# Kernel tuning notes

Measured on AMD Instinct MI355X. Metric: run time of the kernel, lower is better.

The kernel has to match this reference:

```python
import jax, jax.numpy as jnp
import numpy as np

B, T, C = 4, 2048, 1024
E, K, HID = 8, 2, 4096  # n_expert, top-k, mult*dim


def setup_inputs() -> dict:
    key = jax.random.key(0)
    ks = jax.random.split(key, 9)
    s = 1.0 / np.sqrt(C)
    sh = 1.0 / np.sqrt(HID)
    return {
        "x": jax.random.normal(ks[0], (B, T, C), jnp.float32),
        "wg_w": jax.random.normal(ks[1], (C, E), jnp.float32) * s,
        "wg_b": jnp.zeros((E,), jnp.float32),
        "w1": jax.random.normal(ks[2], (E, C, HID), jnp.float32) * s,
        "b1": jnp.zeros((E, HID), jnp.float32),
        "w3": jax.random.normal(ks[3], (E, C, HID), jnp.float32) * s,
        "b3": jnp.zeros((E, HID), jnp.float32),
        "w2": jax.random.normal(ks[4], (E, HID, C), jnp.float32) * sh,
        "b2": jnp.zeros((E, C), jnp.float32),
    }


def reference(x, wg_w, wg_b, w1, b1, w3, b3, w2, b2):
    Bx, Tx, Cx = x.shape
    xf = x.reshape(-1, Cx)                       # (S, C)
    S = xf.shape[0]
    # --- TopKGate ---
    logits = xf @ wg_w + wg_b                    # (S, E)
    probs = jax.nn.softmax(logits, axis=-1)
    vals, idx = jax.lax.top_k(probs, K)          # (S, K)
    importance = probs.mean(axis=0)              # (E,)
    load = jnp.zeros((E,), probs.dtype).at[idx[:, 0]].add(1.0) / S
    aux = E * (importance * load).sum()
    # per-token per-expert combine weight (top-k ids are unique per row)
    w_full = jnp.zeros((S, E), probs.dtype).at[jnp.arange(S)[:, None], idx].add(vals)
    # --- experts: SwiGLU FFN, loop over small fixed E ---
    y = jnp.zeros_like(xf)
    for e in range(E):
        h = jax.nn.silu(xf @ w1[e] + b1[e]) * (xf @ w3[e] + b3[e])  # (S, HID)
        y = y + w_full[:, e:e + 1] * (h @ w2[e] + b2[e])
    return y.reshape(Bx, Tx, Cx), aux
```

## Files before the change

### kernel.cpp

```cpp
#include <hip/hip_runtime.h>

#define S_TOK 8192
#define C_DIM 1024
#define E_NUM 8
#define HID_DIM 4096

typedef unsigned short u16;
typedef __bf16 bf16x8 __attribute__((ext_vector_type(8)));
typedef float f32x4 __attribute__((ext_vector_type(4)));

__device__ __forceinline__ u16 f2bf(float f){
  union { float f; unsigned u; } v; v.f = f;
  unsigned r = v.u + 0x7fffu + ((v.u >> 16) & 1u);
  return (u16)(r >> 16);
}
__device__ __forceinline__ float bf2f(u16 b){
  union { unsigned u; float f; } v; v.u = ((unsigned)b) << 16; return v.f;
}

__device__ __forceinline__ void async_copy16(const void* g, void* l){
  __builtin_amdgcn_global_load_lds((const __attribute__((address_space(1))) void*)g,
                                   (__attribute__((address_space(3))) void*)l, 16, 0, 0);
}

__global__ __launch_bounds__(256) void gate_kernel(
    const float* __restrict__ x, const float* __restrict__ wg_w, const float* __restrict__ wg_b,
    int* __restrict__ top_idx, float* __restrict__ top_val,
    float* __restrict__ imp_sum, int* __restrict__ cnt_top1, int* __restrict__ counts)
{
  __shared__ float s_imp[E_NUM];
  __shared__ int   s_c1[E_NUM], s_cnt[E_NUM];
  if (threadIdx.x < E_NUM){ s_imp[threadIdx.x]=0.f; s_c1[threadIdx.x]=0; s_cnt[threadIdx.x]=0; }
  __syncthreads();

  int wid = threadIdx.x >> 6, lane = threadIdx.x & 63;
  int t = blockIdx.x * 4 + wid;
  const float4* xr4 = (const float4*)(x + (size_t)t * C_DIM);
  float acc[E_NUM];
  #pragma unroll
  for (int e=0;e<E_NUM;e++) acc[e]=0.f;
  #pragma unroll
  for (int c4 = 0; c4 < C_DIM/4/64; c4++){
    int c = (c4*64 + lane);
    float4 xv = xr4[c];
    const float* wr = wg_w + (size_t)c * 4 * E_NUM;
    #pragma unroll
    for (int e=0;e<E_NUM;e++)
      acc[e] += xv.x*wr[e] + xv.y*wr[E_NUM+e] + xv.z*wr[2*E_NUM+e] + xv.w*wr[3*E_NUM+e];
  }
  #pragma unroll
  for (int e=0;e<E_NUM;e++){
    float v = acc[e];
    #pragma unroll
    for (int off=32; off>0; off>>=1) v += __shfl_xor(v, off, 64);
    acc[e] = v + wg_b[e];
  }
  float mx = acc[0];
  #pragma unroll
  for (int e=1;e<E_NUM;e++) mx = fmaxf(mx, acc[e]);
  float sum = 0.f;
  #pragma unroll
  for (int e=0;e<E_NUM;e++){ acc[e] = __expf(acc[e]-mx); sum += acc[e]; }
  float inv = 1.f/sum;
  #pragma unroll
  for (int e=0;e<E_NUM;e++) acc[e] *= inv;
  int i1=0; float v1=acc[0];
  #pragma unroll
  for (int e=1;e<E_NUM;e++) if (acc[e] > v1){ v1=acc[e]; i1=e; }
  int i2=-1; float v2=-1.f;
  #pragma unroll
  for (int e=0;e<E_NUM;e++) if (e!=i1 && acc[e] > v2){ v2=acc[e]; i2=e; }

  if (lane==0){
    top_idx[t*2+0]=i1; top_idx[t*2+1]=i2;
    top_val[t*2+0]=v1; top_val[t*2+1]=v2;
    #pragma unroll
    for (int e=0;e<E_NUM;e++) atomicAdd(&s_imp[e], acc[e]);
    atomicAdd(&s_c1[i1],1);
    atomicAdd(&s_cnt[i1],1); atomicAdd(&s_cnt[i2],1);
  }
  __syncthreads();
  if (threadIdx.x < E_NUM){
    atomicAdd(&imp_sum[threadIdx.x], s_imp[threadIdx.x]);
    atomicAdd(&cnt_top1[threadIdx.x], s_c1[threadIdx.x]);
    atomicAdd(&counts[threadIdx.x], s_cnt[threadIdx.x]);
  }
}

__global__ void scan_kernel(const int* __restrict__ counts, int* __restrict__ offsets,
                            int* __restrict__ cursor, const float* __restrict__ imp_sum,
                            const int* __restrict__ cnt_top1, float* __restrict__ aux_out)
{
  if (threadIdx.x==0 && blockIdx.x==0){
    int off=0;
    #pragma unroll
    for (int e=0;e<E_NUM;e++){ offsets[e]=off; cursor[e]=off; off+=counts[e]; }
    float aux=0.f;
    #pragma unroll
    for (int e=0;e<E_NUM;e++)
      aux += (imp_sum[e]/(float)S_TOK) * ((float)cnt_top1[e]/(float)S_TOK);
    aux_out[0] = aux * (float)E_NUM;
  }
}

__global__ __launch_bounds__(256) void scatter_kernel(
    const int* __restrict__ top_idx, const float* __restrict__ top_val,
    int* __restrict__ cursor, int* __restrict__ token_list, float* __restrict__ token_w,
    int* __restrict__ pos_of_slot)
{
  int t = blockIdx.x*256 + threadIdx.x;
  #pragma unroll
  for (int k=0;k<2;k++){
    int e = top_idx[t*2+k];
    int pos = atomicAdd(&cursor[e], 1);
    token_list[pos] = t;
    token_w[pos]    = top_val[t*2+k];
    pos_of_slot[t*2+k] = pos;
  }
}

__global__ __launch_bounds__(256) void convx_kernel(const float* __restrict__ x, u16* __restrict__ xb){
  const int n4 = S_TOK*C_DIM/4;
  for (int i = blockIdx.x*blockDim.x + threadIdx.x; i < n4; i += gridDim.x*blockDim.x){
    float4 v = ((const float4*)x)[i];
    ushort4 o = make_ushort4(f2bf(v.x), f2bf(v.y), f2bf(v.z), f2bf(v.w));
    ((ushort4*)xb)[i] = o;
  }
}

__global__ __launch_bounds__(256) void transpose_kernel(const float* __restrict__ in, u16* __restrict__ out,
                                                        int R, int Cc)
{
  __shared__ float tile[64][65];
  int e = blockIdx.z;
  const float* src = in  + (size_t)e*R*Cc;
  u16*         dst = out + (size_t)e*R*Cc;
  int c0 = blockIdx.x*64, r0 = blockIdx.y*64;
  int tx = threadIdx.x, ty = threadIdx.y;
  #pragma unroll
  for (int i = ty; i < 64; i += 4)
    tile[i][tx] = src[(size_t)(r0+i)*Cc + c0 + tx];
  __syncthreads();
  #pragma unroll
  for (int i = ty; i < 64; i += 4)
    dst[(size_t)(c0+i)*R + r0 + tx] = f2bf(tile[tx][i]);
}

__global__ __launch_bounds__(512,1) void gemm1_kernel(
    const u16* __restrict__ xb, const u16* __restrict__ w1t, const u16* __restrict__ w3t,
    const float* __restrict__ b1, const float* __restrict__ b3,
    const int* __restrict__ token_list, const int* __restrict__ offsets, const int* __restrict__ counts,
    u16* __restrict__ h)
{
  int e  = blockIdx.z;
  int Ne = counts[e];
  int m0 = blockIdx.y * 128;
  if (m0 >= Ne) return;
  int seg = offsets[e];
  int n0  = blockIdx.x * 128;

  __shared__ u16 lA [128*64];
  __shared__ u16 lB1[128*64];
  __shared__ u16 lB3[128*64];

  int tid = threadIdx.x;
  int wid = tid >> 6, lane = tid & 63;
  int wr = wid >> 2, wc = wid & 3;

  size_t gA[2], gB[2];
  #pragma unroll
  for (int i=0;i<2;i++){
    int r  = wid*16 + i*8 + (lane>>3);
    int rr = m0 + r; if (rr > Ne-1) rr = Ne-1;
    int tok = token_list[seg + rr];
    gA[i] = (size_t)tok * C_DIM + (lane&7)*8;
    int n  = n0 + wid*16 + i*8 + (lane>>3);
    gB[i] = ((size_t)e*HID_DIM + n) * C_DIM + (lane&7)*8;
  }

  f32x4 acc1[4][2], acc3[4][2];
  #pragma unroll
  for (int a=0;a<4;a++)
    #pragma unroll
    for (int b=0;b<2;b++){ acc1[a][b] = (f32x4){0.f,0.f,0.f,0.f}; acc3[a][b] = (f32x4){0.f,0.f,0.f,0.f}; }

  for (int k0=0; k0<C_DIM; k0+=64){
    #pragma unroll
    for (int i=0;i<2;i++){
      int lds_off = (wid*16 + i*8) * 64;
      async_copy16(xb  + gA[i] + k0, &lA [lds_off]);
      async_copy16(w1t + gB[i] + k0, &lB1[lds_off]);
      async_copy16(w3t + gB[i] + k0, &lB3[lds_off]);
    }
    __syncthreads();
    #pragma unroll
    for (int ks=0; ks<2; ks++){
      int kk = ks*32 + (lane>>4)*8;
      bf16x8 af[4], b1f[2], b3f[2];
      #pragma unroll
      for (int mi=0;mi<4;mi++) af[mi]  = *(const bf16x8*)&lA [(wr*64+mi*16+(lane&15))*64 + kk];
      #pragma unroll
      for (int nj=0;nj<2;nj++){ b1f[nj] = *(const bf16x8*)&lB1[(wc*32+nj*16+(lane&15))*64 + kk];
                                b3f[nj] = *(const bf16x8*)&lB3[(wc*32+nj*16+(lane&15))*64 + kk]; }
      #pragma unroll
      for (int mi=0;mi<4;mi++)
        #pragma unroll
        for (int nj=0;nj<2;nj++){
          acc1[mi][nj] = __builtin_amdgcn_mfma_f32_16x16x32_bf16(af[mi], b1f[nj], acc1[mi][nj], 0,0,0);
          acc3[mi][nj] = __builtin_amdgcn_mfma_f32_16x16x32_bf16(af[mi], b3f[nj], acc3[mi][nj], 0,0,0);
        }
    }
    __syncthreads();
  }

  const float* b1p = b1 + (size_t)e*HID_DIM + n0;
  const float* b3p = b3 + (size_t)e*HID_DIM + n0;
  #pragma unroll
  for (int nj=0;nj<2;nj++){
    int nl = wc*32 + nj*16 + (lane&15);
    float bb1 = b1p[nl], bb3 = b3p[nl];
    #pragma unroll
    for (int mi=0;mi<4;mi++){
      #pragma unroll
      for (int r=0;r<4;r++){
        int ml = wr*64 + mi*16 + (lane>>4)*4 + r;
        int m  = m0 + ml;
        if (m < Ne){
          float a = acc1[mi][nj][r] + bb1;
          float b = acc3[mi][nj][r] + bb3;
          float hv = (a / (1.f + __expf(-a))) * b;
          h[(size_t)(seg+m)*HID_DIM + n0 + nl] = f2bf(hv);
        }
      }
    }
  }
}

__global__ __launch_bounds__(256,2) void gemm2_kernel(
    const u16* __restrict__ h, const u16* __restrict__ w2t, const float* __restrict__ b2,
    const float* __restrict__ token_w,
    const int* __restrict__ offsets, const int* __restrict__ counts,
    float* __restrict__ ybuf)
{
  int e  = blockIdx.z;
  int Ne = counts[e];
  int m0 = blockIdx.y * 128;
  if (m0 >= Ne) return;
  int seg = offsets[e];
  int n0  = blockIdx.x * 128;

  __shared__ u16 lA[128*64];
  __shared__ u16 lB[128*64];
  int tid=threadIdx.x, wid=tid>>6, lane=tid&63, wr=wid>>1, wc=wid&1;

  size_t gA[4];
  #pragma unroll
  for (int i=0;i<4;i++){
    int r  = wid*32 + i*8 + (lane>>3);
    int rr = m0 + r; if (rr > Ne-1) rr = Ne-1;
    gA[i] = (size_t)(seg + rr)*HID_DIM + (lane&7)*8;
  }
  size_t gB = ((size_t)e*C_DIM + n0 + wid*32 + (lane>>3)) * HID_DIM + (lane&7)*8;

  f32x4 acc[4][4];
  #pragma unroll
  for (int a=0;a<4;a++)
    #pragma unroll
    for (int b=0;b<4;b++) acc[a][b] = (f32x4){0.f,0.f,0.f,0.f};

  for (int k0=0; k0<HID_DIM; k0+=64){
    #pragma unroll
    for (int i=0;i<4;i++){
      async_copy16(h   + gA[i] + k0,                     &lA[(wid*4+i)*512]);
      async_copy16(w2t + gB + (size_t)i*8*HID_DIM + k0,  &lB[(wid*4+i)*512]);
    }
    __syncthreads();
    #pragma unroll
    for (int ks=0; ks<2; ks++){
      int kk = ks*32 + (lane>>4)*8;
      bf16x8 af[4], bf[4];
      #pragma unroll
      for (int mi=0;mi<4;mi++) af[mi] = *(const bf16x8*)&lA[(wr*64+mi*16+(lane&15))*64 + kk];
      #pragma unroll
      for (int nj=0;nj<4;nj++) bf[nj] = *(const bf16x8*)&lB[(wc*64+nj*16+(lane&15))*64 + kk];
      #pragma unroll
      for (int mi=0;mi<4;mi++)
        #pragma unroll
        for (int nj=0;nj<4;nj++)
          acc[mi][nj] = __builtin_amdgcn_mfma_f32_16x16x32_bf16(af[mi], bf[nj], acc[mi][nj], 0,0,0);
    }
    __syncthreads();
  }

  const float* b2p = b2 + (size_t)e*C_DIM + n0;
  #pragma unroll
  for (int mi=0;mi<4;mi++){
    #pragma unroll
    for (int r=0;r<4;r++){
      int ml = wr*64 + mi*16 + (lane>>4)*4 + r;
      int m  = m0 + ml;
      if (m < Ne){
        float w = token_w[seg+m];
        #pragma unroll
        for (int nj=0;nj<4;nj++){
          int nl = wc*64 + nj*16 + (lane&15);
          ybuf[(size_t)(seg+m)*C_DIM + n0 + nl] = (acc[mi][nj][r] + b2p[nl]) * w;
        }
      }
    }
  }
}

__global__ __launch_bounds__(256) void combine_kernel(
    const float* __restrict__ ybuf, const int* __restrict__ pos_of_slot, float* __restrict__ y)
{
  int t = blockIdx.x;
  int p0 = pos_of_slot[t*2+0], p1 = pos_of_slot[t*2+1];
  const float4* a = (const float4*)(ybuf + (size_t)p0*C_DIM);
  const float4* b = (const float4*)(ybuf + (size_t)p1*C_DIM);
  float4* o = (float4*)(y + (size_t)t*C_DIM);
  int c = threadIdx.x;
  float4 va = a[c], vb = b[c];
  o[c] = make_float4(va.x+vb.x, va.y+vb.y, va.z+vb.z, va.w+vb.w);
}

extern "C" void kernel_launch(void* const* d_in, const int* in_sizes, int n_in,
                              void* d_out, int out_size, void* d_ws, size_t ws_size,
                              hipStream_t stream)
{
  const float* x    = (const float*)d_in[0];
  const float* wg_w = (const float*)d_in[1];
  const float* wg_b = (const float*)d_in[2];
  const float* w1   = (const float*)d_in[3];
  const float* b1   = (const float*)d_in[4];
  const float* w3   = (const float*)d_in[5];
  const float* b3   = (const float*)d_in[6];
  const float* w2   = (const float*)d_in[7];
  const float* b2   = (const float*)d_in[8];

  float* y   = (float*)d_out;
  float* aux = y + (size_t)S_TOK*C_DIM;

  char* ws = (char*)d_ws;
  size_t off = 0;
  auto alloc = [&](size_t bytes) -> void* {
    void* p = ws + off;
    off += (bytes + 255) & ~(size_t)255;
    return p;
  };
  u16*  xb        = (u16*)  alloc((size_t)S_TOK*C_DIM*2);
  u16*  w1t       = (u16*)  alloc((size_t)E_NUM*HID_DIM*C_DIM*2);
  u16*  w3t       = (u16*)  alloc((size_t)E_NUM*HID_DIM*C_DIM*2);
  u16*  w2t       = (u16*)  alloc((size_t)E_NUM*C_DIM*HID_DIM*2);
  u16*  h         = (u16*)  alloc((size_t)S_TOK*2*HID_DIM*2);
  int*  token_list= (int*)  alloc((size_t)S_TOK*2*4);
  float* token_w  = (float*)alloc((size_t)S_TOK*2*4);
  int*  top_idx   = (int*)  alloc((size_t)S_TOK*2*4);
  float* top_val  = (float*)alloc((size_t)S_TOK*2*4);
  int*  pos_of_slot=(int*)  alloc((size_t)S_TOK*2*4);
  char* stats     = (char*) alloc(4096);
  float* imp_sum  = (float*)(stats);
  int*   cnt1     = (int*)  (stats + 64);
  int*   counts   = (int*)  (stats + 128);
  int*   offsets  = (int*)  (stats + 192);
  int*   cursor   = (int*)  (stats + 256);
  float* ybuf = (float*)w1t;
  (void)in_sizes; (void)n_in; (void)out_size; (void)ws_size;

  hipMemsetAsync(stats, 0, 512, stream);

  convx_kernel<<<2048, 256, 0, stream>>>(x, xb);
  dim3 tb(64,4);
  transpose_kernel<<<dim3(HID_DIM/64, C_DIM/64, E_NUM), tb, 0, stream>>>(w1, w1t, C_DIM, HID_DIM);
  transpose_kernel<<<dim3(HID_DIM/64, C_DIM/64, E_NUM), tb, 0, stream>>>(w3, w3t, C_DIM, HID_DIM);
  transpose_kernel<<<dim3(C_DIM/64, HID_DIM/64, E_NUM), tb, 0, stream>>>(w2, w2t, HID_DIM, C_DIM);

  gate_kernel<<<S_TOK/4, 256, 0, stream>>>(x, wg_w, wg_b, top_idx, top_val, imp_sum, cnt1, counts);
  scan_kernel<<<1, 64, 0, stream>>>(counts, offsets, cursor, imp_sum, cnt1, aux);
  scatter_kernel<<<S_TOK/256, 256, 0, stream>>>(top_idx, top_val, cursor, token_list, token_w, pos_of_slot);

  gemm1_kernel<<<dim3(HID_DIM/128, S_TOK/128, E_NUM), 512, 0, stream>>>(
      xb, w1t, w3t, b1, b3, token_list, offsets, counts, h);
  gemm2_kernel<<<dim3(C_DIM/128, S_TOK/128, E_NUM), 256, 0, stream>>>(
      h, w2t, b2, token_w, offsets, counts, ybuf);
  combine_kernel<<<S_TOK, 256, 0, stream>>>(ybuf, pos_of_slot, y);
}
```

Measured before the change: 931.8 us.

## Swizzle LDS tiles, widen gemm2 to 8 waves, bf16 ybuf, vectorize transpose

The gemm1 and gemm2 LDS tiles now use an XOR swizzle. It is applied to the global source offset of each async copy and to the k-offset of each fragment read, to cut LDS bank conflicts on the bf16x8 loads. gemm2 moves from 4 waves with 4x4 MFMA tiles to 8 waves with 4x2 tiles, one block per CU. The intermediate expert outputs are stored as bf16 instead of fp32, which halves ybuf traffic in gemm2 and combine at some cost in precision. The weight transpose uses float2 loads and ushort2 stores with a 32x8 thread block.

New measurement: 831.8 us. 10.7% less time.

```diff
diff --git a/kernel.cpp b/kernel.cpp
--- a/kernel.cpp
+++ b/kernel.cpp
@@ -138,13 +138,18 @@
   int c0 = blockIdx.x*64, r0 = blockIdx.y*64;
   int tx = threadIdx.x, ty = threadIdx.y;
   #pragma unroll
-  for (int i = ty; i < 64; i += 4)
-    tile[i][tx] = src[(size_t)(r0+i)*Cc + c0 + tx];
+  for (int i = ty; i < 64; i += 8){
+    float2 v = *(const float2*)&src[(size_t)(r0+i)*Cc + c0 + tx*2];
+    tile[i][tx*2+0] = v.x; tile[i][tx*2+1] = v.y;
+  }
   __syncthreads();
   #pragma unroll
-  for (int i = ty; i < 64; i += 4)
-    dst[(size_t)(c0+i)*R + r0 + tx] = f2bf(tile[tx][i]);
-}
+  for (int i = ty; i < 64; i += 8){
+    ushort2 o = make_ushort2(f2bf(tile[tx*2+0][i]), f2bf(tile[tx*2+1][i]));
+    *(ushort2*)&dst[(size_t)(c0+i)*R + r0 + tx*2] = o;
+  }
+}
+
 
 __global__ __launch_bounds__(512,1) void gemm1_kernel(
     const u16* __restrict__ xb, const u16* __restrict__ w1t, const u16* __restrict__ w3t,
@@ -167,15 +172,17 @@
   int wid = tid >> 6, lane = tid & 63;
   int wr = wid >> 2, wc = wid & 3;
 
+  const int srcsw = (((lane&7) ^ ((lane>>3)&7))) * 8;
+
   size_t gA[2], gB[2];
   #pragma unroll
   for (int i=0;i<2;i++){
     int r  = wid*16 + i*8 + (lane>>3);
     int rr = m0 + r; if (rr > Ne-1) rr = Ne-1;
     int tok = token_list[seg + rr];
-    gA[i] = (size_t)tok * C_DIM + (lane&7)*8;
+    gA[i] = (size_t)tok * C_DIM + srcsw;
     int n  = n0 + wid*16 + i*8 + (lane>>3);
-    gB[i] = ((size_t)e*HID_DIM + n) * C_DIM + (lane&7)*8;
+    gB[i] = ((size_t)e*HID_DIM + n) * C_DIM + srcsw;
   }
 
   f32x4 acc1[4][2], acc3[4][2];
@@ -195,13 +202,13 @@
     __syncthreads();
     #pragma unroll
     for (int ks=0; ks<2; ks++){
-      int kk = ks*32 + (lane>>4)*8;
+      int kkS = ((ks*4 + (lane>>4)) ^ (lane&7)) * 8;
       bf16x8 af[4], b1f[2], b3f[2];
       #pragma unroll
-      for (int mi=0;mi<4;mi++) af[mi]  = *(const bf16x8*)&lA [(wr*64+mi*16+(lane&15))*64 + kk];
-      #pragma unroll
-      for (int nj=0;nj<2;nj++){ b1f[nj] = *(const bf16x8*)&lB1[(wc*32+nj*16+(lane&15))*64 + kk];
-                                b3f[nj] = *(const bf16x8*)&lB3[(wc*32+nj*16+(lane&15))*64 + kk]; }
+      for (int mi=0;mi<4;mi++) af[mi]  = *(const bf16x8*)&lA [(wr*64+mi*16+(lane&15))*64 + kkS];
+      #pragma unroll
+      for (int nj=0;nj<2;nj++){ b1f[nj] = *(const bf16x8*)&lB1[(wc*32+nj*16+(lane&15))*64 + kkS];
+                                b3f[nj] = *(const bf16x8*)&lB3[(wc*32+nj*16+(lane&15))*64 + kkS]; }
       #pragma unroll
       for (int mi=0;mi<4;mi++)
         #pragma unroll
@@ -236,11 +243,11 @@
   }
 }
 
-__global__ __launch_bounds__(256,2) void gemm2_kernel(
+__global__ __launch_bounds__(512,1) void gemm2_kernel(
     const u16* __restrict__ h, const u16* __restrict__ w2t, const float* __restrict__ b2,
     const float* __restrict__ token_w,
     const int* __restrict__ offsets, const int* __restrict__ counts,
-    float* __restrict__ ybuf)
+    u16* __restrict__ ybuf)
 {
   int e  = blockIdx.z;
   int Ne = counts[e];
@@ -251,42 +258,46 @@
 
   __shared__ u16 lA[128*64];
   __shared__ u16 lB[128*64];
-  int tid=threadIdx.x, wid=tid>>6, lane=tid&63, wr=wid>>1, wc=wid&1;
-
-  size_t gA[4];
-  #pragma unroll
-  for (int i=0;i<4;i++){
-    int r  = wid*32 + i*8 + (lane>>3);
+  int tid=threadIdx.x, wid=tid>>6, lane=tid&63, wr=wid>>2, wc=wid&3;
+
+  const int srcsw = (((lane&7) ^ ((lane>>3)&7))) * 8;
+
+  size_t gA[2], gB[2];
+  #pragma unroll
+  for (int i=0;i<2;i++){
+    int r  = wid*16 + i*8 + (lane>>3);
     int rr = m0 + r; if (rr > Ne-1) rr = Ne-1;
-    gA[i] = (size_t)(seg + rr)*HID_DIM + (lane&7)*8;
-  }
-  size_t gB = ((size_t)e*C_DIM + n0 + wid*32 + (lane>>3)) * HID_DIM + (lane&7)*8;
-
-  f32x4 acc[4][4];
+    gA[i] = (size_t)(seg + rr)*HID_DIM + srcsw;
+    int n  = n0 + wid*16 + i*8 + (lane>>3);
+    gB[i] = ((size_t)e*C_DIM + n) * HID_DIM + srcsw;
+  }
+
+  f32x4 acc[4][2];
   #pragma unroll
   for (int a=0;a<4;a++)
     #pragma unroll
-    for (int b=0;b<4;b++) acc[a][b] = (f32x4){0.f,0.f,0.f,0.f};
+    for (int b=0;b<2;b++) acc[a][b] = (f32x4){0.f,0.f,0.f,0.f};
 
   for (int k0=0; k0<HID_DIM; k0+=64){
     #pragma unroll
-    for (int i=0;i<4;i++){
-      async_copy16(h   + gA[i] + k0,                     &lA[(wid*4+i)*512]);
-      async_copy16(w2t + gB + (size_t)i*8*HID_DIM + k0,  &lB[(wid*4+i)*512]);
+    for (int i=0;i<2;i++){
+      int lds_off = (wid*16 + i*8) * 64;
+      async_copy16(h   + gA[i] + k0, &lA[lds_off]);
+      async_copy16(w2t + gB[i] + k0, &lB[lds_off]);
     }
     __syncthreads();
     #pragma unroll
     for (int ks=0; ks<2; ks++){
-      int kk = ks*32 + (lane>>4)*8;
-      bf16x8 af[4], bf[4];
-      #pragma unroll
-      for (int mi=0;mi<4;mi++) af[mi] = *(const bf16x8*)&lA[(wr*64+mi*16+(lane&15))*64 + kk];
-      #pragma unroll
-      for (int nj=0;nj<4;nj++) bf[nj] = *(const bf16x8*)&lB[(wc*64+nj*16+(lane&15))*64 + kk];
+      int kkS = ((ks*4 + (lane>>4)) ^ (lane&7)) * 8;
+      bf16x8 af[4], bf[2];
+      #pragma unroll
+      for (int mi=0;mi<4;mi++) af[mi] = *(const bf16x8*)&lA[(wr*64+mi*16+(lane&15))*64 + kkS];
+      #pragma unroll
+      for (int nj=0;nj<2;nj++) bf[nj] = *(const bf16x8*)&lB[(wc*32+nj*16+(lane&15))*64 + kkS];
       #pragma unroll
       for (int mi=0;mi<4;mi++)
         #pragma unroll
-        for (int nj=0;nj<4;nj++)
+        for (int nj=0;nj<2;nj++)
           acc[mi][nj] = __builtin_amdgcn_mfma_f32_16x16x32_bf16(af[mi], bf[nj], acc[mi][nj], 0,0,0);
     }
     __syncthreads();
@@ -302,9 +313,9 @@
       if (m < Ne){
         float w = token_w[seg+m];
         #pragma unroll
-        for (int nj=0;nj<4;nj++){
-          int nl = wc*64 + nj*16 + (lane&15);
-          ybuf[(size_t)(seg+m)*C_DIM + n0 + nl] = (acc[mi][nj][r] + b2p[nl]) * w;
+        for (int nj=0;nj<2;nj++){
+          int nl = wc*32 + nj*16 + (lane&15);
+          ybuf[(size_t)(seg+m)*C_DIM + n0 + nl] = f2bf((acc[mi][nj][r] + b2p[nl]) * w);
         }
       }
     }
@@ -312,16 +323,16 @@
 }
 
 __global__ __launch_bounds__(256) void combine_kernel(
-    const float* __restrict__ ybuf, const int* __restrict__ pos_of_slot, float* __restrict__ y)
+    const u16* __restrict__ ybuf, const int* __restrict__ pos_of_slot, float* __restrict__ y)
 {
   int t = blockIdx.x;
   int p0 = pos_of_slot[t*2+0], p1 = pos_of_slot[t*2+1];
-  const float4* a = (const float4*)(ybuf + (size_t)p0*C_DIM);
-  const float4* b = (const float4*)(ybuf + (size_t)p1*C_DIM);
-  float4* o = (float4*)(y + (size_t)t*C_DIM);
   int c = threadIdx.x;
-  float4 va = a[c], vb = b[c];
-  o[c] = make_float4(va.x+vb.x, va.y+vb.y, va.z+vb.z, va.w+vb.w);
+  ushort4 a = ((const ushort4*)(ybuf + (size_t)p0*C_DIM))[c];
+  ushort4 b = ((const ushort4*)(ybuf + (size_t)p1*C_DIM))[c];
+  float4 o = make_float4(bf2f(a.x)+bf2f(b.x), bf2f(a.y)+bf2f(b.y),
+                         bf2f(a.z)+bf2f(b.z), bf2f(a.w)+bf2f(b.w));
+  ((float4*)(y + (size_t)t*C_DIM))[c] = o;
 }
 
 extern "C" void kernel_launch(void* const* d_in, const int* in_sizes, int n_in,
@@ -364,13 +375,13 @@
   int*   counts   = (int*)  (stats + 128);
   int*   offsets  = (int*)  (stats + 192);
   int*   cursor   = (int*)  (stats + 256);
-  float* ybuf = (float*)w1t;
+  u16* ybuf = (u16*)w1t;
   (void)in_sizes; (void)n_in; (void)out_size; (void)ws_size;
 
   hipMemsetAsync(stats, 0, 512, stream);
 
   convx_kernel<<<2048, 256, 0, stream>>>(x, xb);
-  dim3 tb(64,4);
+  dim3 tb(32,8);
   transpose_kernel<<<dim3(HID_DIM/64, C_DIM/64, E_NUM), tb, 0, stream>>>(w1, w1t, C_DIM, HID_DIM);
   transpose_kernel<<<dim3(HID_DIM/64, C_DIM/64, E_NUM), tb, 0, stream>>>(w3, w3t, C_DIM, HID_DIM);
   transpose_kernel<<<dim3(C_DIM/64, HID_DIM/64, E_NUM), tb, 0, stream>>>(w2, w2t, HID_DIM, C_DIM);
@@ -381,7 +392,7 @@
 
   gemm1_kernel<<<dim3(HID_DIM/128, S_TOK/128, E_NUM), 512, 0, stream>>>(
       xb, w1t, w3t, b1, b3, token_list, offsets, counts, h);
-  gemm2_kernel<<<dim3(C_DIM/128, S_TOK/128, E_NUM), 256, 0, stream>>>(
+  gemm2_kernel<<<dim3(C_DIM/128, S_TOK/128, E_NUM), 512, 0, stream>>>(
       h, w2t, b2, token_w, offsets, counts, ybuf);
   combine_kernel<<<S_TOK, 256, 0, stream>>>(ybuf, pos_of_slot, y);
 }
```
